# Optimization experiments

Measured on AMD Instinct MI355X. Metric: run time of the kernel, lower is better.

The kernel has to match this reference:

```python
import jax, jax.numpy as jnp
import numpy as np

SHIFT = 1  # shift_direction fixed to +1 (original picks +/-1 randomly at init)


def setup_inputs() -> dict:
    key = jax.random.key(0)
    k1, k2 = jax.random.split(key)
    x = jax.random.normal(k1, (1, 64, 56, 56), dtype=jnp.float32)
    W = jax.random.normal(k2, (64, 3, 2, 64), dtype=jnp.float32)
    return {"x": x, "W": W}


def reference(x, W):
    # permute 'ijkl -> iljk' and flatten (j,k) -> columns: (1,1,56,3584)
    t2 = jnp.transpose(x, (0, 3, 1, 2)).reshape(1, 1, 56, 3584)
    # unfold kernel (3,1), padding (1,0): three vertically shifted copies with zero pad
    pad = jnp.pad(t2, ((0, 0), (0, 0), (1, 1), (0, 0)))
    taps = jnp.stack([pad[:, 0, t:t + 56, :] for t in range(3)], axis=1)  # (1,3,56,3584)
    taps = taps.reshape(1, 3, 56, 64, 56)  # (m, tap k, o=orig-l, j=channels, n=orig-k)
    # contract taps (k=3) and channels (j=64) against weight (i,k,l,j)
    t3 = jnp.einsum('mkojn,iklj->mioln', taps, W)  # (1,64,56,2,56)
    # merge (o,l)->112, circular roll, split back, sum over the pair dim
    t4 = t3.reshape(1, 64, 112, 56)
    t4 = jnp.roll(t4, SHIFT, axis=2)
    t4 = t4.reshape(1, 64, 56, 2, 56).sum(axis=3)  # (1,64,56,56)
    # final circular roll along last spatial axis
    return jnp.roll(t4, SHIFT, axis=3)
```

## Files before the change

kernel.cpp:

```cpp
#include <hip/hip_runtime.h>

#define SP 56
#define CH 64
#define XSTRIDE 3136

__global__ void tsc_prep(const float* __restrict__ W, float4* __restrict__ Cv) {
  int u = blockIdx.x * blockDim.x + threadIdx.x;
  if (u >= CH * CH) return;
  int j = u & 63;
  int i = u >> 6;
  const float* Wi = W + i * 384 + j;
  float w00 = Wi[0];
  float w01 = Wi[64];
  float w10 = Wi[128];
  float w11 = Wi[192];
  float w20 = Wi[256];
  float w21 = Wi[320];
  Cv[j * 64 + i]        = make_float4(w01, w00 + w11, w10 + w21, w20);
  Cv[4096 + j * 64 + i] = make_float4(w10, w20, w01, w11);
}

__global__ __launch_bounds__(256) void tsc_main(const float* __restrict__ x,
                                                const float4* __restrict__ Cv,
                                                float* __restrict__ out) {
  __shared__ float xs[CH][8];
  __shared__ float red[4][2][64];

  const int t  = threadIdx.x;
  const int i  = t & 63;
  const int w  = t >> 6;
  const int op = blockIdx.x;
  const int n  = blockIdx.y;
  const int o0 = op * 2;
  const int ns = (n + SP - 1) % SP;

  const float* xrow = x + ns * SP;
#pragma unroll
  for (int k = 0; k < 2; ++k) {
    int u = t + k * 256;
    int j = u >> 3;
    int b = u & 7;
    int g = o0 - 2 + b;
    if (g < 0) g += SP;
    float v = (g < SP) ? xrow[j * XSTRIDE + g] : 0.f;
    xs[j][b] = v;
  }
  __syncthreads();

  float a0 = 0.f, a1 = 0.f;
  const float4* cb = Cv + i;
  const int j0 = w * 16;

  if (op != 0) {
#pragma unroll 4
    for (int jj = 0; jj < 16; ++jj) {
      int j = j0 + jj;
      float4 c = cb[j * 64];
      float x0 = xs[j][0], x1 = xs[j][1], x2 = xs[j][2];
      float x3 = xs[j][3], x4 = xs[j][4];
      a0 += c.x * x0 + c.y * x1 + c.z * x2 + c.w * x3;
      a1 += c.x * x1 + c.y * x2 + c.z * x3 + c.w * x4;
    }
  } else {
#pragma unroll 4
    for (int jj = 0; jj < 16; ++jj) {
      int j = j0 + jj;
      float4 c = cb[j * 64];
      float4 d = cb[4096 + j * 64];
      float x0 = xs[j][0], x1 = xs[j][1], x2 = xs[j][2];
      float x3 = xs[j][3], x4 = xs[j][4];
      a0 += d.x * x2 + d.y * x3 + d.z * x0 + d.w * x1;
      a1 += c.y * x2 + c.z * x3 + c.w * x4;
    }
  }

  red[w][0][i] = a0;
  red[w][1][i] = a1;
  __syncthreads();

  if (t < 128) {
    int s  = t >> 6;
    int ii = t & 63;
    float v = red[0][s][ii] + red[1][s][ii] + red[2][s][ii] + red[3][s][ii];
    out[ii * XSTRIDE + (o0 + s) * SP + n] = v;
  }
}

extern "C" void kernel_launch(void* const* d_in, const int* in_sizes, int n_in,
                              void* d_out, int out_size, void* d_ws, size_t ws_size,
                              hipStream_t stream) {
  const float* x = (const float*)d_in[0];
  const float* W = (const float*)d_in[1];
  float* out = (float*)d_out;
  float4* Cv = (float4*)d_ws;

  tsc_prep<<<dim3(16), dim3(256), 0, stream>>>(W, Cv);
  tsc_main<<<dim3(28, 56), dim3(256), 0, stream>>>(x, Cv, out);
}
```

Measured before the change: 63.58 us.

## Compute four output rows per block and prefetch weights into registers

Each block now produces four o-rows instead of two, which halves the grid and doubles reuse of the weight float4s loaded per thread. Those weights are preloaded into a register array before the barrier so the global loads overlap with the shared-memory staging of x. Shared reads of x become float4 vector loads, and the launch bounds add an occupancy hint. The cost is higher register pressure and fewer blocks in flight.

```diff
diff --git a/kernel.cpp b/kernel.cpp
--- a/kernel.cpp
+++ b/kernel.cpp
@@ -20,18 +20,18 @@
   Cv[4096 + j * 64 + i] = make_float4(w10, w20, w01, w11);
 }
 
-__global__ __launch_bounds__(256) void tsc_main(const float* __restrict__ x,
-                                                const float4* __restrict__ Cv,
-                                                float* __restrict__ out) {
-  __shared__ float xs[CH][8];
-  __shared__ float red[4][2][64];
+__global__ __launch_bounds__(256, 4) void tsc_main(const float* __restrict__ x,
+                                                   const float4* __restrict__ Cv,
+                                                   float* __restrict__ out) {
+  __shared__ __align__(16) float xs[CH][8];
+  __shared__ float red[4][4][64];
 
   const int t  = threadIdx.x;
   const int i  = t & 63;
   const int w  = t >> 6;
-  const int op = blockIdx.x;
+  const int oq = blockIdx.x;
   const int n  = blockIdx.y;
-  const int o0 = op * 2;
+  const int o0 = oq * 4;
   const int ns = (n + SP - 1) % SP;
 
   const float* xrow = x + ns * SP;
@@ -45,40 +45,53 @@
     float v = (g < SP) ? xrow[j * XSTRIDE + g] : 0.f;
     xs[j][b] = v;
   }
+
+  const int j0 = w * 16;
+  const float4* cb = Cv + i;
+  float4 c[16];
+#pragma unroll
+  for (int jj = 0; jj < 16; ++jj) c[jj] = cb[(j0 + jj) * 64];
+
   __syncthreads();
 
-  float a0 = 0.f, a1 = 0.f;
-  const float4* cb = Cv + i;
-  const int j0 = w * 16;
+  float a0 = 0.f, a1 = 0.f, a2 = 0.f, a3 = 0.f;
 
-  if (op != 0) {
-#pragma unroll 4
+  if (oq != 0) {
+#pragma unroll
     for (int jj = 0; jj < 16; ++jj) {
       int j = j0 + jj;
-      float4 c = cb[j * 64];
-      float x0 = xs[j][0], x1 = xs[j][1], x2 = xs[j][2];
-      float x3 = xs[j][3], x4 = xs[j][4];
-      a0 += c.x * x0 + c.y * x1 + c.z * x2 + c.w * x3;
-      a1 += c.x * x1 + c.y * x2 + c.z * x3 + c.w * x4;
+      const float4* xv = (const float4*)xs[j];
+      float4 xA = xv[0];
+      float4 xB = xv[1];
+      float4 cc = c[jj];
+      a0 += cc.x * xA.x + cc.y * xA.y + cc.z * xA.z + cc.w * xA.w;
+      a1 += cc.x * xA.y + cc.y * xA.z + cc.z * xA.w + cc.w * xB.x;
+      a2 += cc.x * xA.z + cc.y * xA.w + cc.z * xB.x + cc.w * xB.y;
+      a3 += cc.x * xA.w + cc.y * xB.x + cc.z * xB.y + cc.w * xB.z;
     }
   } else {
 #pragma unroll 4
     for (int jj = 0; jj < 16; ++jj) {
       int j = j0 + jj;
-      float4 c = cb[j * 64];
-      float4 d = cb[4096 + j * 64];
-      float x0 = xs[j][0], x1 = xs[j][1], x2 = xs[j][2];
-      float x3 = xs[j][3], x4 = xs[j][4];
-      a0 += d.x * x2 + d.y * x3 + d.z * x0 + d.w * x1;
-      a1 += c.y * x2 + c.z * x3 + c.w * x4;
+      const float4* xv = (const float4*)xs[j];
+      float4 xA = xv[0];
+      float4 xB = xv[1];
+      float4 cc = c[jj];
+      float4 d  = cb[4096 + j * 64];
+      a0 += d.x * xA.z + d.y * xA.w + d.z * xA.x + d.w * xA.y;
+      a1 += cc.y * xA.z + cc.z * xA.w + cc.w * xB.x;
+      a2 += cc.x * xA.z + cc.y * xA.w + cc.z * xB.x + cc.w * xB.y;
+      a3 += cc.x * xA.w + cc.y * xB.x + cc.z * xB.y + cc.w * xB.z;
     }
   }
 
   red[w][0][i] = a0;
   red[w][1][i] = a1;
+  red[w][2][i] = a2;
+  red[w][3][i] = a3;
   __syncthreads();
 
-  if (t < 128) {
+  {
     int s  = t >> 6;
     int ii = t & 63;
     float v = red[0][s][ii] + red[1][s][ii] + red[2][s][ii] + red[3][s][ii];
@@ -95,5 +108,5 @@
   float4* Cv = (float4*)d_ws;
 
   tsc_prep<<<dim3(16), dim3(256), 0, stream>>>(W, Cv);
-  tsc_main<<<dim3(28, 56), dim3(256), 0, stream>>>(x, Cv, out);
+  tsc_main<<<dim3(14, 56), dim3(256), 0, stream>>>(x, Cv, out);
 }
```

After: 89.09 us. 40.1% more time.

## Compute one output row per block with 128 threads and float4 LDS reads

Applied to the files above, without the earlier changes.

Restructures the main kernel so each block computes a single output row position with 128 threads (two warps splitting 32 channels each) instead of two rows with 256 threads, doubling the grid. Each thread prefetches the first eight weight vectors before the barrier, reads the input window as one aligned float4 from shared memory, and keeps four independent accumulators. Boundary handling is split into o==0, o==1 and general cases. This targets barrier, LDS and reduction overhead and improves latency hiding, but loses the reuse of each weight load across two output rows, so total weight traffic doubles.

```diff
diff --git a/kernel.cpp b/kernel.cpp
--- a/kernel.cpp
+++ b/kernel.cpp
@@ -20,70 +20,79 @@
   Cv[4096 + j * 64 + i] = make_float4(w10, w20, w01, w11);
 }
 
-__global__ __launch_bounds__(256) void tsc_main(const float* __restrict__ x,
+__global__ __launch_bounds__(128) void tsc_main(const float* __restrict__ x,
                                                 const float4* __restrict__ Cv,
                                                 float* __restrict__ out) {
-  __shared__ float xs[CH][8];
-  __shared__ float red[4][2][64];
+  __shared__ __align__(16) float xs[CH][4];
+  __shared__ float red[64];
 
-  const int t  = threadIdx.x;
-  const int i  = t & 63;
-  const int w  = t >> 6;
-  const int op = blockIdx.x;
-  const int n  = blockIdx.y;
-  const int o0 = op * 2;
+  const int t = threadIdx.x;
+  const int i = t & 63;
+  const int w = t >> 6;
+  const int o = blockIdx.x;
+  const int n = blockIdx.y;
   const int ns = (n + SP - 1) % SP;
 
   const float* xrow = x + ns * SP;
 #pragma unroll
   for (int k = 0; k < 2; ++k) {
-    int u = t + k * 256;
-    int j = u >> 3;
-    int b = u & 7;
-    int g = o0 - 2 + b;
+    int u = t + k * 128;
+    int j = u >> 2;
+    int b = u & 3;
+    int g = o - 2 + b;
     if (g < 0) g += SP;
-    float v = (g < SP) ? xrow[j * XSTRIDE + g] : 0.f;
-    xs[j][b] = v;
+    xs[j][b] = (g < SP) ? xrow[j * XSTRIDE + g] : 0.f;
   }
+
+  const int j0 = w * 32;
+  const float4* cb = Cv + i;
+  float4 p0 = cb[(j0 + 0) * 64];
+  float4 p1 = cb[(j0 + 1) * 64];
+  float4 p2 = cb[(j0 + 2) * 64];
+  float4 p3 = cb[(j0 + 3) * 64];
+  float4 p4 = cb[(j0 + 4) * 64];
+  float4 p5 = cb[(j0 + 5) * 64];
+  float4 p6 = cb[(j0 + 6) * 64];
+  float4 p7 = cb[(j0 + 7) * 64];
+
   __syncthreads();
 
-  float a0 = 0.f, a1 = 0.f;
-  const float4* cb = Cv + i;
-  const int j0 = w * 16;
+  float a0 = 0.f, a1 = 0.f, a2 = 0.f, a3 = 0.f;
 
-  if (op != 0) {
-#pragma unroll 4
-    for (int jj = 0; jj < 16; ++jj) {
-      int j = j0 + jj;
-      float4 c = cb[j * 64];
-      float x0 = xs[j][0], x1 = xs[j][1], x2 = xs[j][2];
-      float x3 = xs[j][3], x4 = xs[j][4];
-      a0 += c.x * x0 + c.y * x1 + c.z * x2 + c.w * x3;
-      a1 += c.x * x1 + c.y * x2 + c.z * x3 + c.w * x4;
+#define GSTEP(cc, jv) { const float4 xv = *(const float4*)(xs[jv]);            \
+    a0 += (cc).x * xv.x; a1 += (cc).y * xv.y;                                  \
+    a2 += (cc).z * xv.z; a3 += (cc).w * xv.w; }
+
+  if (o >= 2) {
+    GSTEP(p0, j0 + 0) GSTEP(p1, j0 + 1) GSTEP(p2, j0 + 2) GSTEP(p3, j0 + 3)
+    GSTEP(p4, j0 + 4) GSTEP(p5, j0 + 5) GSTEP(p6, j0 + 6) GSTEP(p7, j0 + 7)
+#pragma unroll 8
+    for (int jj = 8; jj < 32; ++jj) {
+      const float4 cc = cb[(j0 + jj) * 64];
+      GSTEP(cc, j0 + jj)
+    }
+  } else if (o == 1) {
+#pragma unroll 8
+    for (int jj = 0; jj < 32; ++jj) {
+      const float4 cc = cb[(j0 + jj) * 64];
+      const float4 xv = *(const float4*)(xs[j0 + jj]);
+      a1 += cc.y * xv.y; a2 += cc.z * xv.z; a3 += cc.w * xv.w;
     }
   } else {
-#pragma unroll 4
-    for (int jj = 0; jj < 16; ++jj) {
-      int j = j0 + jj;
-      float4 c = cb[j * 64];
-      float4 d = cb[4096 + j * 64];
-      float x0 = xs[j][0], x1 = xs[j][1], x2 = xs[j][2];
-      float x3 = xs[j][3], x4 = xs[j][4];
-      a0 += d.x * x2 + d.y * x3 + d.z * x0 + d.w * x1;
-      a1 += c.y * x2 + c.z * x3 + c.w * x4;
+#pragma unroll 8
+    for (int jj = 0; jj < 32; ++jj) {
+      const float4 d = cb[4096 + (j0 + jj) * 64];
+      const float4 xv = *(const float4*)(xs[j0 + jj]);
+      a0 += d.x * xv.z; a1 += d.y * xv.w; a2 += d.z * xv.x; a3 += d.w * xv.y;
     }
   }
+#undef GSTEP
 
-  red[w][0][i] = a0;
-  red[w][1][i] = a1;
+  const float v = a0 + a1 + a2 + a3;
+
+  if (w == 1) red[i] = v;
   __syncthreads();
-
-  if (t < 128) {
-    int s  = t >> 6;
-    int ii = t & 63;
-    float v = red[0][s][ii] + red[1][s][ii] + red[2][s][ii] + red[3][s][ii];
-    out[ii * XSTRIDE + (o0 + s) * SP + n] = v;
-  }
+  if (w == 0) out[i * XSTRIDE + o * SP + n] = v + red[i];
 }
 
 extern "C" void kernel_launch(void* const* d_in, const int* in_sizes, int n_in,
@@ -95,5 +104,5 @@
   float4* Cv = (float4*)d_ws;
 
   tsc_prep<<<dim3(16), dim3(256), 0, stream>>>(W, Cv);
-  tsc_main<<<dim3(28, 56), dim3(256), 0, stream>>>(x, Cv, out);
+  tsc_main<<<dim3(56, 56), dim3(128), 0, stream>>>(x, Cv, out);
 }
```

Result: slower. 65.08 us (+2.4%).

## Fuse weight prep into main kernel, compute four rows per block

Applied to the files above, without the earlier changes.

Removes the separate weight-preprocessing kernel and its launch. Each block now builds the combined weight coefficients for one half of the output channels directly in shared memory. Each thread computes four output rows instead of two, using vectorized shared loads of x and a wave-shuffle partial reduction, and the grid is reshaped to 14x56x2. The cost is that every block reloads and recombines W slices from global memory, adding redundant work per block, plus extra global W reads in the boundary branch.

```diff
diff --git a/kernel.cpp b/kernel.cpp
--- a/kernel.cpp
+++ b/kernel.cpp
@@ -4,85 +4,101 @@
 #define CH 64
 #define XSTRIDE 3136
 
-__global__ void tsc_prep(const float* __restrict__ W, float4* __restrict__ Cv) {
-  int u = blockIdx.x * blockDim.x + threadIdx.x;
-  if (u >= CH * CH) return;
-  int j = u & 63;
-  int i = u >> 6;
-  const float* Wi = W + i * 384 + j;
-  float w00 = Wi[0];
-  float w01 = Wi[64];
-  float w10 = Wi[128];
-  float w11 = Wi[192];
-  float w20 = Wi[256];
-  float w21 = Wi[320];
-  Cv[j * 64 + i]        = make_float4(w01, w00 + w11, w10 + w21, w20);
-  Cv[4096 + j * 64 + i] = make_float4(w10, w20, w01, w11);
-}
-
-__global__ __launch_bounds__(256) void tsc_main(const float* __restrict__ x,
-                                                const float4* __restrict__ Cv,
-                                                float* __restrict__ out) {
-  __shared__ float xs[CH][8];
-  __shared__ float red[4][2][64];
+__global__ __launch_bounds__(256, 4) void tsc_fused(const float* __restrict__ x,
+                                                    const float* __restrict__ W,
+                                                    float* __restrict__ out) {
+  __shared__ __align__(16) float4 Cw[CH][33];
+  __shared__ __align__(16) float  xs[CH][8];
+  __shared__ float red[4][4][32];
 
   const int t  = threadIdx.x;
-  const int i  = t & 63;
-  const int w  = t >> 6;
-  const int op = blockIdx.x;
+  const int ob = blockIdx.x;
   const int n  = blockIdx.y;
-  const int o0 = op * 2;
+  const int h  = blockIdx.z;
+  const int o0 = ob * 4;
   const int ns = (n + SP - 1) % SP;
 
-  const float* xrow = x + ns * SP;
+  {
+    const int j  = t & 63;
+    const int ig = t >> 6;
 #pragma unroll
-  for (int k = 0; k < 2; ++k) {
-    int u = t + k * 256;
-    int j = u >> 3;
-    int b = u & 7;
-    int g = o0 - 2 + b;
-    if (g < 0) g += SP;
-    float v = (g < SP) ? xrow[j * XSTRIDE + g] : 0.f;
-    xs[j][b] = v;
+    for (int q = 0; q < 8; ++q) {
+      const int il = ig * 8 + q;
+      const float* Wp = W + (h * 32 + il) * 384 + j;
+      float w00 = Wp[0],   w01 = Wp[64],  w10 = Wp[128];
+      float w11 = Wp[192], w20 = Wp[256], w21 = Wp[320];
+      Cw[j][il] = make_float4(w01, w00 + w11, w10 + w21, w20);
+    }
+  }
+
+  {
+    const float* xrow = x + ns * SP;
+#pragma unroll
+    for (int k = 0; k < 2; ++k) {
+      int u = t + k * 256;
+      int j = u >> 3;
+      int b = u & 7;
+      int g = o0 - 2 + b;
+      if (g < 0) g += SP;
+      xs[j][b] = (g < SP) ? xrow[j * XSTRIDE + g] : 0.f;
+    }
   }
   __syncthreads();
 
-  float a0 = 0.f, a1 = 0.f;
-  const float4* cb = Cv + i;
-  const int j0 = w * 16;
+  const int il = t & 31;
+  const int jh = (t >> 5) & 1;
+  const int w  = t >> 6;
+  const int jbase = w * 16 + jh * 8;
 
-  if (op != 0) {
-#pragma unroll 4
-    for (int jj = 0; jj < 16; ++jj) {
-      int j = j0 + jj;
-      float4 c = cb[j * 64];
-      float x0 = xs[j][0], x1 = xs[j][1], x2 = xs[j][2];
-      float x3 = xs[j][3], x4 = xs[j][4];
-      a0 += c.x * x0 + c.y * x1 + c.z * x2 + c.w * x3;
-      a1 += c.x * x1 + c.y * x2 + c.z * x3 + c.w * x4;
+  float a0 = 0.f, a1 = 0.f, a2 = 0.f, a3 = 0.f;
+
+  if (ob != 0) {
+#pragma unroll
+    for (int jj = 0; jj < 8; ++jj) {
+      const int j = jbase + jj;
+      const float4 c  = Cw[j][il];
+      const float4 xA = *(const float4*)&xs[j][0];
+      const float4 xB = *(const float4*)&xs[j][4];
+      a0 += c.x * xA.x + c.y * xA.y + c.z * xA.z + c.w * xA.w;
+      a1 += c.x * xA.y + c.y * xA.z + c.z * xA.w + c.w * xB.x;
+      a2 += c.x * xA.z + c.y * xA.w + c.z * xB.x + c.w * xB.y;
+      a3 += c.x * xA.w + c.y * xB.x + c.z * xB.y + c.w * xB.z;
     }
   } else {
-#pragma unroll 4
-    for (int jj = 0; jj < 16; ++jj) {
-      int j = j0 + jj;
-      float4 c = cb[j * 64];
-      float4 d = cb[4096 + j * 64];
-      float x0 = xs[j][0], x1 = xs[j][1], x2 = xs[j][2];
-      float x3 = xs[j][3], x4 = xs[j][4];
-      a0 += d.x * x2 + d.y * x3 + d.z * x0 + d.w * x1;
-      a1 += c.y * x2 + c.z * x3 + c.w * x4;
+    const float* Wg = W + (h * 32 + il) * 384;
+#pragma unroll
+    for (int jj = 0; jj < 8; ++jj) {
+      const int j = jbase + jj;
+      const float w10 = Wg[128 + j];
+      const float w11 = Wg[192 + j];
+      const float4 c  = Cw[j][il];
+      const float4 xA = *(const float4*)&xs[j][0];
+      const float4 xB = *(const float4*)&xs[j][4];
+      a0 += c.x * xA.x + w11 * xA.y + w10 * xA.z + c.w * xA.w;
+      a1 +=              c.y * xA.z + c.z * xA.w + c.w * xB.x;
+      a2 += c.x * xA.z + c.y * xA.w + c.z * xB.x + c.w * xB.y;
+      a3 += c.x * xA.w + c.y * xB.x + c.z * xB.y + c.w * xB.z;
     }
   }
 
-  red[w][0][i] = a0;
-  red[w][1][i] = a1;
+  a0 += __shfl_down(a0, 32);
+  a1 += __shfl_down(a1, 32);
+  a2 += __shfl_down(a2, 32);
+  a3 += __shfl_down(a3, 32);
+
+  if ((t & 63) < 32) {
+    red[w][0][il] = a0;
+    red[w][1][il] = a1;
+    red[w][2][il] = a2;
+    red[w][3][il] = a3;
+  }
   __syncthreads();
 
   if (t < 128) {
-    int s  = t >> 6;
-    int ii = t & 63;
-    float v = red[0][s][ii] + red[1][s][ii] + red[2][s][ii] + red[3][s][ii];
-    out[ii * XSTRIDE + (o0 + s) * SP + n] = v;
+    const int r  = t >> 5;
+    const int ii = t & 31;
+    const float v = red[0][r][ii] + red[1][r][ii] + red[2][r][ii] + red[3][r][ii];
+    out[(h * 32 + ii) * XSTRIDE + (o0 + r) * SP + n] = v;
   }
 }
 
@@ -92,8 +108,7 @@
   const float* x = (const float*)d_in[0];
   const float* W = (const float*)d_in[1];
   float* out = (float*)d_out;
-  float4* Cv = (float4*)d_ws;
+  (void)d_ws; (void)ws_size;
 
-  tsc_prep<<<dim3(16), dim3(256), 0, stream>>>(W, Cv);
-  tsc_main<<<dim3(28, 56), dim3(256), 0, stream>>>(x, Cv, out);
+  tsc_fused<<<dim3(14, 56, 2), dim3(256), 0, stream>>>(x, W, out);
 }
```

Result: no change. 62.39 us (-1.9%).
